# Performance work log

Measured on AMD Instinct MI355X. Metric: run time of the kernel, lower is better.

Reference implementation:

```python
import jax, jax.numpy as jnp
import numpy as np

FEAT_STRIDE = 16
SCORE_THRESH = 0.7
DIST_THRESH = 16.0
MAX_OUT = 50
B = 2048
IMG_W = 65536


def setup_inputs() -> dict:
    key = jax.random.key(0)
    k1, k2, k3 = jax.random.split(key, 3)
    fw = IMG_W // FEAT_STRIDE
    pred_cls_logit = jax.random.normal(k1, (B, fw), dtype=jnp.float32)
    pred_delta = jax.random.normal(k2, (B, fw, 2), dtype=jnp.float32)
    # realistic image widths in [0.5, 1.0] * img_width
    real_images_width = jax.random.uniform(k3, (B,), jnp.float32, 0.5, 1.0) * IMG_W
    return {
        "pred_cls_logit": pred_cls_logit,
        "pred_delta": pred_delta,
        "img_width": IMG_W,
        "real_images_width": real_images_width,
    }


def _nms_one(positions, scores):
    # positions: [N, 2], scores: [N]. Greedy 1D NMS, fixed MAX_OUT iterations.
    centers = positions.mean(axis=1)                      # [N]
    alive0 = scores >= SCORE_THRESH                       # score-threshold filter

    def step(alive, _):
        masked = jnp.where(alive, scores, -1e30)
        i = jnp.argmax(masked)                            # highest remaining score
        has = jnp.any(alive)
        f = has.astype(jnp.float32)                       # 1.0 if a box was picked
        p = positions[i] * f
        s = scores[i] * f
        # suppress everything within DIST_THRESH of picked center (incl. itself)
        new_alive = alive & (jnp.abs(centers - centers[i]) > DIST_THRESH)
        return new_alive, (p, s, f)

    _, (P, S, F) = jax.lax.scan(step, alive0, None, length=MAX_OUT)
    # pad_to_fixed_size: append validity flag column, zero-padded rows
    nms_positions = jnp.concatenate([P, F[:, None]], axis=1)   # [MAX_OUT, 3]
    nms_scores = jnp.concatenate([S[:, None], F[:, None]], axis=1)  # [MAX_OUT, 2]
    return nms_positions, nms_scores


def reference(pred_cls_logit, pred_delta, img_width, real_images_width):
    feat_width = img_width // FEAT_STRIDE
    interval_center = (jnp.arange(feat_width, dtype=jnp.float32) + 0.5) * FEAT_STRIDE
    # [B, feat_width, 2]
    pos = pred_delta * FEAT_STRIDE + interval_center[None, :, None]
    scores = jax.nn.sigmoid(pred_cls_logit)               # [B, feat_width]
    max_width = real_images_width[:, None, None] - 1.0
    pos = jnp.where(pos < 0.0, 0.0, pos)
    pos = jnp.where(pos > max_width, max_width, pos)

    nms_positions, nms_scores = jax.vmap(_nms_one)(pos, scores)

    nms_center = nms_positions[..., :2].mean(axis=2)      # [B, MAX_OUT]
    x_interval_num = jnp.floor(nms_center / FEAT_STRIDE).astype(jnp.int32)
    valid = nms_positions[..., 2] == 1.0
    idx = jnp.where(valid, x_interval_num, feat_width)    # out-of-range -> dropped
    cls_ids = jax.vmap(
        lambda ii: jnp.zeros((feat_width,), jnp.float32).at[ii].set(1.0, mode='drop')
    )(idx)                                                # [B, feat_width]
    return nms_positions, nms_scores, cls_ids
```

## Files before the change

kernel.cpp:

```cpp
#include <hip/hip_runtime.h>
#include <math.h>

#define FW 4096
#define MAX_OUT 50
#define WCAP 320
#define NSLOT 1024
#define T0 0.885f
#define SELCAP 128


__global__ __launch_bounds__(256) void essp_k1(
    const float* __restrict__ logits,
    const float* __restrict__ deltas,
    const float* __restrict__ realw,
    float* stage)
{
  __shared__ float Lx[4][WCAP];
  __shared__ int   Li[4][WCAP];
  __shared__ int   Lcnt[4];
  __shared__ int   Lsel, Lalv;

  const int row  = blockIdx.x;
  const int tid  = threadIdx.x;
  const int lane = tid & 63;
  const int w    = tid >> 6;

  if (tid == 0) { Lsel = 0; Lalv = 0; }

  const float mw = realw[row] - 1.0f;
  const float* lgr = logits + (size_t)row * FW;
  const float* dlr = deltas + (size_t)row * (2 * FW);
  const unsigned long long below = (1ULL << lane) - 1ULL;

  int cnt = 0;
  #pragma unroll
  for (int r = 0; r < 4; ++r) {
    const int i0 = w * 1024 + r * 256 + 4 * lane;
    const float4 lx = *(const float4*)(lgr + i0);
    const float xs[4] = {lx.x, lx.y, lx.z, lx.w};
    bool c4[4]; unsigned long long m4[4];
    #pragma unroll
    for (int e = 0; e < 4; ++e) { c4[e] = (xs[e] >= 0.846f); m4[e] = __ballot(c4[e]); }
    int base = cnt + __popcll(m4[0] & below) + __popcll(m4[1] & below)
                   + __popcll(m4[2] & below) + __popcll(m4[3] & below);
    int off = 0;
    #pragma unroll
    for (int e = 0; e < 4; ++e) {
      if (c4[e]) {
        const int slot = base + off;
        if (slot < WCAP) { Lx[w][slot] = xs[e]; Li[w][slot] = i0 + e; }
        ++off;
      }
    }
    cnt += __popcll(m4[0]) + __popcll(m4[1]) + __popcll(m4[2]) + __popcll(m4[3]);
  }
  if (lane == 0) Lcnt[w] = (cnt < WCAP) ? cnt : WCAP;
  __syncthreads();

  const int c0 = Lcnt[0], c1 = Lcnt[1], c2 = Lcnt[2], c3 = Lcnt[3];
  const int p1 = c0, p2 = c0 + c1, p3 = c0 + c1 + c2;
  int nc = p3 + c3; nc = (nc < NSLOT) ? nc : NSLOT;

  float* Srow = stage + (size_t)row * FW;
  unsigned short* idxrow = (unsigned short*)(Srow + 2048);
  unsigned long long* keyrow = (unsigned long long*)(Srow + 2560);

  #pragma unroll
  for (int g0 = 0; g0 < NSLOT; g0 += 256) {
    const int g = g0 + tid;
    float score = -1e30f, cen = 0.0f;
    int idx = 0;
    if (g < nc) {
      const int wsel = (g >= p1) + (g >= p2) + (g >= p3);
      int pre = 0;
      pre = (wsel == 1) ? p1 : pre;
      pre = (wsel == 2) ? p2 : pre;
      pre = (wsel == 3) ? p3 : pre;
      const int kk = g - pre;
      const float x = (&Lx[0][0])[wsel * WCAP + kk];
      idx = (&Li[0][0])[wsel * WCAP + kk];
      const float2 d = *(const float2*)(dlr + 2 * idx);
      const float ic = ((float)idx + 0.5f) * 16.0f;
      float q0 = d.x * 16.0f + ic;
      float q1 = d.y * 16.0f + ic;
      q0 = (q0 < 0.f) ? 0.f : q0;  q0 = (q0 > mw) ? mw : q0;
      q1 = (q1 < 0.f) ? 0.f : q1;  q1 = (q1 > mw) ? mw : q1;
      cen = (q0 + q1) * 0.5f;
      const float s = (float)(1.0 / (1.0 + exp(-(double)x)));
      score = (s >= 0.7f) ? s : -1e30f;
    }
    Srow[g]        = score;
    Srow[1024 + g] = cen;
    idxrow[g]      = (unsigned short)idx;

    const unsigned long long am = __ballot(score >= 0.7f);
    if (lane == 0) atomicAdd(&Lalv, __popcll(am));
    const unsigned long long sm = __ballot(score >= T0);
    int sbase = 0;
    if (lane == 0 && sm) sbase = atomicAdd(&Lsel, __popcll(sm));
    sbase = __shfl(sbase, 0, 64);
    if (score >= T0) {
      const int pos = sbase + __popcll(sm & below);
      if (pos < SELCAP) {
        keyrow[pos] = (((unsigned long long)__float_as_uint(score)) << 11)
                      | (unsigned)(2047 - g);
        Srow[2816 + pos] = cen;
      }
    }
  }
  __syncthreads();
  if (tid == 0) {
    *(int*)(Srow + 2944) = Lsel;
    *(int*)(Srow + 2945) = Lalv;
  }
}

#define KDEF(J, SS, CE)                                                       \
  const unsigned kb##J = ((SS) >= 0.7f) ? __float_as_uint(SS) : 0u;           \
  const float c##J = (CE);

#define INIT1F(J, SLOTEXPR)                                                   \
  unsigned long long fk##J = kb##J                                            \
      ? ((((unsigned long long)kb##J) << 11) | (unsigned)(2047 - (SLOTEXPR))) \
      : 0ULL;

#define M2(RK, RC, KA, CA, KB, CB)                                            \
  const bool t##RK = (KB) > (KA);                                             \
  const unsigned long long RK = t##RK ? (KB) : (KA);                          \
  const float RC = t##RK ? (CB) : (CA);

#define BSTEP(CTRL) {                                                         \
  const unsigned lo_ = (unsigned)__builtin_amdgcn_update_dpp(                 \
      (int)(unsigned)bk, (int)(unsigned)bk, CTRL, 0xF, 0xF, false);           \
  const unsigned hi_ = (unsigned)__builtin_amdgcn_update_dpp(                 \
      (int)(unsigned)(bk >> 32), (int)(unsigned)(bk >> 32), CTRL, 0xF, 0xF,   \
      false);                                                                 \
  const float oc_ = __int_as_float(__builtin_amdgcn_update_dpp(               \
      __float_as_int(bc), __float_as_int(bc), CTRL, 0xF, 0xF, false));        \
  const unsigned long long ok_ = ((unsigned long long)hi_ << 32) | lo_;       \
  const bool tb_ = ok_ > bk;                                                  \
  bk = tb_ ? ok_ : bk;  bc = tb_ ? oc_ : bc; }

#define SUPF(J) {                                                             \
  const bool ts_ = fabsf(c##J - wc) <= 16.0f;                                 \
  fk##J = ts_ ? 0ULL : fk##J; }

__global__ __launch_bounds__(64) void essp_k2(
    const float* __restrict__ deltas,
    const float* __restrict__ realw,
    float* out_pos,
    float* out_scr,
    float* cls_all)
{
  const int row  = blockIdx.x;
  const int lane = threadIdx.x;
  const int l4   = 4 * lane;
  float* Srow = cls_all + (size_t)row * FW;

  const int sel = *(const int*)(Srow + 2944);
  const int alv = *(const int*)(Srow + 2945);

  int pkv = -1;
  float psv = 0.f;
  bool need_heavy = (sel > SELCAP);

  if (!need_heavy) {
    const unsigned long long* kp = (const unsigned long long*)(Srow + 2560);
    unsigned long long ka = (lane < sel)      ? kp[lane]      : 0ULL;
    unsigned long long kb = (lane + 64 < sel) ? kp[lane + 64] : 0ULL;
    const float ca = (lane < sel)      ? Srow[2816 + lane]      : 0.f;
    const float cb = (lane + 64 < sel) ? Srow[2816 + 64 + lane] : 0.f;

    int cacc = 0;
    #pragma unroll 1
    for (int it = 0; it < MAX_OUT; ++it) {
      const bool tm = kb > ka;
      unsigned long long bk = tm ? kb : ka;
      float bc = tm ? cb : ca;
      BSTEP(0xB1)
      BSTEP(0x4E)
      BSTEP(0x141)
      BSTEP(0x140)
      BSTEP(0x142)
      BSTEP(0x143)
      const unsigned rhi = (unsigned)__builtin_amdgcn_readlane(
          (int)(unsigned)(bk >> 32), 63);
      const unsigned rlo = (unsigned)__builtin_amdgcn_readlane(
          (int)(unsigned)bk, 63);
      const float rc = __int_as_float(
          __builtin_amdgcn_readlane(__float_as_int(bc), 63));
      const unsigned sbits = (rhi << 21) | (rlo >> 11);
      if (sbits == 0u) break;
      if (lane == it) {
        pkv = 2047 - (int)(rlo & 0x7FFu);
        psv = __uint_as_float(sbits);
      }
      ++cacc;
      const float wc = rc;
      if (fabsf(ca - wc) <= 16.0f) ka = 0ULL;
      if (fabsf(cb - wc) <= 16.0f) kb = 0ULL;
    }
    if (cacc < MAX_OUT && alv > sel) { need_heavy = true; pkv = -1; psv = 0.f; }
  }

  if (need_heavy) {
    const float4 s4a = *(const float4*)(Srow + l4);
    const float4 s4b = *(const float4*)(Srow + 256 + l4);
    const float4 s4c = *(const float4*)(Srow + 512 + l4);
    const float4 s4d = *(const float4*)(Srow + 768 + l4);
    const float4 e4a = *(const float4*)(Srow + 1024 + l4);
    const float4 e4b = *(const float4*)(Srow + 1280 + l4);
    const float4 e4c = *(const float4*)(Srow + 1536 + l4);
    const float4 e4d = *(const float4*)(Srow + 1792 + l4);

    KDEF(0,  s4a.x, e4a.x)  KDEF(1,  s4a.y, e4a.y)
    KDEF(2,  s4a.z, e4a.z)  KDEF(3,  s4a.w, e4a.w)
    KDEF(4,  s4b.x, e4b.x)  KDEF(5,  s4b.y, e4b.y)
    KDEF(6,  s4b.z, e4b.z)  KDEF(7,  s4b.w, e4b.w)
    KDEF(8,  s4c.x, e4c.x)  KDEF(9,  s4c.y, e4c.y)
    KDEF(10, s4c.z, e4c.z)  KDEF(11, s4c.w, e4c.w)
    KDEF(12, s4d.x, e4d.x)  KDEF(13, s4d.y, e4d.y)
    KDEF(14, s4d.z, e4d.z)  KDEF(15, s4d.w, e4d.w)

    INIT1F(0,  l4 + 0)       INIT1F(1,  l4 + 1)       INIT1F(2,  l4 + 2)
    INIT1F(3,  l4 + 3)       INIT1F(4,  256 + l4 + 0) INIT1F(5,  256 + l4 + 1)
    INIT1F(6,  256 + l4 + 2) INIT1F(7,  256 + l4 + 3) INIT1F(8,  512 + l4 + 0)
    INIT1F(9,  512 + l4 + 1) INIT1F(10, 512 + l4 + 2) INIT1F(11, 512 + l4 + 3)
    INIT1F(12, 768 + l4 + 0) INIT1F(13, 768 + l4 + 1) INIT1F(14, 768 + l4 + 2)
    INIT1F(15, 768 + l4 + 3)

    #pragma unroll 1
    for (int it = 0; it < MAX_OUT; ++it) {
      M2(ka0, ca0, fk0,  c0,  fk1,  c1)
      M2(ka1, ca1, fk2,  c2,  fk3,  c3)
      M2(ka2, ca2, fk4,  c4,  fk5,  c5)
      M2(ka3, ca3, fk6,  c6,  fk7,  c7)
      M2(ka4, ca4, fk8,  c8,  fk9,  c9)
      M2(ka5, ca5, fk10, c10, fk11, c11)
      M2(ka6, ca6, fk12, c12, fk13, c13)
      M2(ka7, ca7, fk14, c14, fk15, c15)
      M2(kb0, cb0, ka0, ca0, ka1, ca1)
      M2(kb1, cb1, ka2, ca2, ka3, ca3)
      M2(kb2, cb2, ka4, ca4, ka5, ca5)
      M2(kb3, cb3, ka6, ca6, ka7, ca7)
      M2(kc0, cc0, kb0, cb0, kb1, cb1)
      M2(kc1, cc1, kb2, cb2, kb3, cb3)
      M2(kd0, cd0, kc0, cc0, kc1, cc1)

      unsigned long long bk = kd0;
      float bc = cd0;
      BSTEP(0xB1) BSTEP(0x4E) BSTEP(0x141) BSTEP(0x140) BSTEP(0x142) BSTEP(0x143)

      const unsigned rhi = (unsigned)__builtin_amdgcn_readlane(
          (int)(unsigned)(bk >> 32), 63);
      const unsigned rlo = (unsigned)__builtin_amdgcn_readlane(
          (int)(unsigned)bk, 63);
      const float rc = __int_as_float(
          __builtin_amdgcn_readlane(__float_as_int(bc), 63));
      const unsigned sbits = (rhi << 21) | (rlo >> 11);
      const bool valid = sbits != 0u;
      const float wc = valid ? rc : 3.0e38f;
      if (lane == it) {
        pkv = valid ? (2047 - (int)(rlo & 0x7FFu)) : -1;
        psv = __uint_as_float(sbits);
      }
      SUPF(0)  SUPF(1)  SUPF(2)  SUPF(3)  SUPF(4)  SUPF(5)  SUPF(6)  SUPF(7)
      SUPF(8)  SUPF(9)  SUPF(10) SUPF(11) SUPF(12) SUPF(13) SUPF(14) SUPF(15)
    }
  }

  float p0 = 0.f, p1 = 0.f;
  int ci = -1;
  if (pkv >= 0) {
    const int idx = ((const unsigned short*)(Srow + 2048))[pkv];
    const float2 d = *(const float2*)(deltas + (size_t)row * (2 * FW) + 2 * idx);
    const float mw = realw[row] - 1.0f;
    const float ic = ((float)idx + 0.5f) * 16.0f;
    p0 = d.x * 16.0f + ic;
    p1 = d.y * 16.0f + ic;
    p0 = (p0 < 0.f) ? 0.f : p0;  p0 = (p0 > mw) ? mw : p0;
    p1 = (p1 < 0.f) ? 0.f : p1;  p1 = (p1 > mw) ? mw : p1;
    ci = (int)floorf(((p0 + p1) * 0.5f) * 0.0625f);
  }
  asm volatile("s_waitcnt vmcnt(0)" ::: "memory");

  const float4 z4 = make_float4(0.f, 0.f, 0.f, 0.f);
  #pragma unroll
  for (int q = 0; q < 16; ++q)
    *(float4*)(Srow + 256 * q + l4) = z4;
  asm volatile("s_waitcnt vmcnt(0)" ::: "memory");

  float* prow = out_pos + (size_t)row * (MAX_OUT * 3);
  float* srow = out_scr + (size_t)row * (MAX_OUT * 2);
  if (lane < MAX_OUT) {
    if (pkv >= 0) {
      prow[3 * lane + 0] = p0;
      prow[3 * lane + 1] = p1;
      prow[3 * lane + 2] = 1.0f;
      srow[2 * lane + 0] = psv;
      srow[2 * lane + 1] = 1.0f;
      if (ci >= 0 && ci < FW) Srow[ci] = 1.0f;
    } else {
      prow[3 * lane + 0] = 0.0f;
      prow[3 * lane + 1] = 0.0f;
      prow[3 * lane + 2] = 0.0f;
      srow[2 * lane + 0] = 0.0f;
      srow[2 * lane + 1] = 0.0f;
    }
  }
}

extern "C" void kernel_launch(void* const* d_in, const int* in_sizes, int n_in,
                              void* d_out, int out_size, void* d_ws, size_t ws_size,
                              hipStream_t stream) {
  const float* logits = (const float*)d_in[0];
  const float* deltas = (const float*)d_in[1];
  const float* realw  = (const float*)d_in[3];
  const int Bn = in_sizes[3];
  float* out_pos = (float*)d_out;
  float* out_scr = out_pos + (size_t)Bn * MAX_OUT * 3;
  float* out_cls = out_scr + (size_t)Bn * MAX_OUT * 2;

  essp_k1<<<Bn, 256, 0, stream>>>(logits, deltas, realw, out_cls);
  essp_k2<<<Bn, 64, 0, stream>>>(deltas, realw, out_pos, out_scr, out_cls);
}
```

Baseline: 77.23 us.

## Fuse candidate-extraction and NMS kernels into one block using shared memory

Merges the two kernels so that scores, centers, indices and the selection keys stay in LDS instead of being staged through the cls output buffer in global memory. The cls row is zeroed at kernel start, and only wave 0 goes on to run the greedy NMS after the barrier. This removes a launch, the global staging round trip and the separate zeroing pass after NMS. In exchange, LDS per block grows, which may lower occupancy, and three of the four waves sit idle during the serial NMS phase.

New measurement: 84.14 us. 9.0% more time.

```diff
diff --git a/kernel.cpp b/kernel.cpp
--- a/kernel.cpp
+++ b/kernel.cpp
@@ -8,17 +8,53 @@
 #define T0 0.885f
 #define SELCAP 128
 
-
-__global__ __launch_bounds__(256) void essp_k1(
+#define KDEF(J, SS, CE)                                                       \
+  const unsigned kb##J = ((SS) >= 0.7f) ? __float_as_uint(SS) : 0u;           \
+  const float c##J = (CE);
+
+#define INIT1F(J, SLOTEXPR)                                                   \
+  unsigned long long fk##J = kb##J                                            \
+      ? ((((unsigned long long)kb##J) << 11) | (unsigned)(2047 - (SLOTEXPR))) \
+      : 0ULL;
+
+#define M2(RK, RC, KA, CA, KB, CB)                                            \
+  const bool t##RK = (KB) > (KA);                                             \
+  const unsigned long long RK = t##RK ? (KB) : (KA);                          \
+  const float RC = t##RK ? (CB) : (CA);
+
+#define BSTEP(CTRL) {                                                         \
+  const unsigned lo_ = (unsigned)__builtin_amdgcn_update_dpp(                 \
+      (int)(unsigned)bk, (int)(unsigned)bk, CTRL, 0xF, 0xF, false);           \
+  const unsigned hi_ = (unsigned)__builtin_amdgcn_update_dpp(                 \
+      (int)(unsigned)(bk >> 32), (int)(unsigned)(bk >> 32), CTRL, 0xF, 0xF,   \
+      false);                                                                 \
+  const float oc_ = __int_as_float(__builtin_amdgcn_update_dpp(               \
+      __float_as_int(bc), __float_as_int(bc), CTRL, 0xF, 0xF, false));        \
+  const unsigned long long ok_ = ((unsigned long long)hi_ << 32) | lo_;       \
+  const bool tb_ = ok_ > bk;                                                  \
+  bk = tb_ ? ok_ : bk;  bc = tb_ ? oc_ : bc; }
+
+#define SUPF(J) {                                                             \
+  const bool ts_ = fabsf(c##J - wc) <= 16.0f;                                 \
+  fk##J = ts_ ? 0ULL : fk##J; }
+
+__global__ __launch_bounds__(256) void essp_fused(
     const float* __restrict__ logits,
     const float* __restrict__ deltas,
     const float* __restrict__ realw,
-    float* stage)
+    float* __restrict__ out_pos,
+    float* __restrict__ out_scr,
+    float* __restrict__ out_cls)
 {
   __shared__ float Lx[4][WCAP];
   __shared__ int   Li[4][WCAP];
   __shared__ int   Lcnt[4];
-  __shared__ int   Lsel, Lalv;
+  __shared__ __align__(16) float Lsc[NSLOT];
+  __shared__ __align__(16) float Lce[NSLOT];
+  __shared__ unsigned short Lidx[NSLOT];
+  __shared__ unsigned long long Lkey[SELCAP];
+  __shared__ float Lc2[SELCAP];
+  __shared__ int Lsel, Lalv;
 
   const int row  = blockIdx.x;
   const int tid  = threadIdx.x;
@@ -30,7 +66,14 @@
   const float mw = realw[row] - 1.0f;
   const float* lgr = logits + (size_t)row * FW;
   const float* dlr = deltas + (size_t)row * (2 * FW);
+  float* cls = out_cls + (size_t)row * FW;
   const unsigned long long below = (1ULL << lane) - 1ULL;
+
+  {
+    const float4 z = make_float4(0.f, 0.f, 0.f, 0.f);
+    #pragma unroll
+    for (int r = 0; r < 4; ++r) *(float4*)(cls + 1024 * r + 4 * tid) = z;
+  }
 
   int cnt = 0;
   #pragma unroll
@@ -58,12 +101,8 @@
   __syncthreads();
 
   const int c0 = Lcnt[0], c1 = Lcnt[1], c2 = Lcnt[2], c3 = Lcnt[3];
-  const int p1 = c0, p2 = c0 + c1, p3 = c0 + c1 + c2;
-  int nc = p3 + c3; nc = (nc < NSLOT) ? nc : NSLOT;
-
-  float* Srow = stage + (size_t)row * FW;
-  unsigned short* idxrow = (unsigned short*)(Srow + 2048);
-  unsigned long long* keyrow = (unsigned long long*)(Srow + 2560);
+  const int pw1 = c0, pw2 = c0 + c1, pw3 = c0 + c1 + c2;
+  int nc = pw3 + c3; nc = (nc < NSLOT) ? nc : NSLOT;
 
   #pragma unroll
   for (int g0 = 0; g0 < NSLOT; g0 += 256) {
@@ -71,11 +110,11 @@
     float score = -1e30f, cen = 0.0f;
     int idx = 0;
     if (g < nc) {
-      const int wsel = (g >= p1) + (g >= p2) + (g >= p3);
+      const int wsel = (g >= pw1) + (g >= pw2) + (g >= pw3);
       int pre = 0;
-      pre = (wsel == 1) ? p1 : pre;
-      pre = (wsel == 2) ? p2 : pre;
-      pre = (wsel == 3) ? p3 : pre;
+      pre = (wsel == 1) ? pw1 : pre;
+      pre = (wsel == 2) ? pw2 : pre;
+      pre = (wsel == 3) ? pw3 : pre;
       const int kk = g - pre;
       const float x = (&Lx[0][0])[wsel * WCAP + kk];
       idx = (&Li[0][0])[wsel * WCAP + kk];
@@ -89,9 +128,9 @@
       const float s = (float)(1.0 / (1.0 + exp(-(double)x)));
       score = (s >= 0.7f) ? s : -1e30f;
     }
-    Srow[g]        = score;
-    Srow[1024 + g] = cen;
-    idxrow[g]      = (unsigned short)idx;
+    Lsc[g]  = score;
+    Lce[g]  = cen;
+    Lidx[g] = (unsigned short)idx;
 
     const unsigned long long am = __ballot(score >= 0.7f);
     if (lane == 0) atomicAdd(&Lalv, __popcll(am));
@@ -102,74 +141,25 @@
     if (score >= T0) {
       const int pos = sbase + __popcll(sm & below);
       if (pos < SELCAP) {
-        keyrow[pos] = (((unsigned long long)__float_as_uint(score)) << 11)
-                      | (unsigned)(2047 - g);
-        Srow[2816 + pos] = cen;
+        Lkey[pos] = (((unsigned long long)__float_as_uint(score)) << 11)
+                    | (unsigned)(2047 - g);
+        Lc2[pos] = cen;
       }
     }
   }
   __syncthreads();
-  if (tid == 0) {
-    *(int*)(Srow + 2944) = Lsel;
-    *(int*)(Srow + 2945) = Lalv;
-  }
-}
-
-#define KDEF(J, SS, CE)                                                       \
-  const unsigned kb##J = ((SS) >= 0.7f) ? __float_as_uint(SS) : 0u;           \
-  const float c##J = (CE);
-
-#define INIT1F(J, SLOTEXPR)                                                   \
-  unsigned long long fk##J = kb##J                                            \
-      ? ((((unsigned long long)kb##J) << 11) | (unsigned)(2047 - (SLOTEXPR))) \
-      : 0ULL;
-
-#define M2(RK, RC, KA, CA, KB, CB)                                            \
-  const bool t##RK = (KB) > (KA);                                             \
-  const unsigned long long RK = t##RK ? (KB) : (KA);                          \
-  const float RC = t##RK ? (CB) : (CA);
-
-#define BSTEP(CTRL) {                                                         \
-  const unsigned lo_ = (unsigned)__builtin_amdgcn_update_dpp(                 \
-      (int)(unsigned)bk, (int)(unsigned)bk, CTRL, 0xF, 0xF, false);           \
-  const unsigned hi_ = (unsigned)__builtin_amdgcn_update_dpp(                 \
-      (int)(unsigned)(bk >> 32), (int)(unsigned)(bk >> 32), CTRL, 0xF, 0xF,   \
-      false);                                                                 \
-  const float oc_ = __int_as_float(__builtin_amdgcn_update_dpp(               \
-      __float_as_int(bc), __float_as_int(bc), CTRL, 0xF, 0xF, false));        \
-  const unsigned long long ok_ = ((unsigned long long)hi_ << 32) | lo_;       \
-  const bool tb_ = ok_ > bk;                                                  \
-  bk = tb_ ? ok_ : bk;  bc = tb_ ? oc_ : bc; }
-
-#define SUPF(J) {                                                             \
-  const bool ts_ = fabsf(c##J - wc) <= 16.0f;                                 \
-  fk##J = ts_ ? 0ULL : fk##J; }
-
-__global__ __launch_bounds__(64) void essp_k2(
-    const float* __restrict__ deltas,
-    const float* __restrict__ realw,
-    float* out_pos,
-    float* out_scr,
-    float* cls_all)
-{
-  const int row  = blockIdx.x;
-  const int lane = threadIdx.x;
-  const int l4   = 4 * lane;
-  float* Srow = cls_all + (size_t)row * FW;
-
-  const int sel = *(const int*)(Srow + 2944);
-  const int alv = *(const int*)(Srow + 2945);
-
+  if (w != 0) return;
+
+  const int sel = Lsel, alv = Lalv;
   int pkv = -1;
   float psv = 0.f;
   bool need_heavy = (sel > SELCAP);
 
   if (!need_heavy) {
-    const unsigned long long* kp = (const unsigned long long*)(Srow + 2560);
-    unsigned long long ka = (lane < sel)      ? kp[lane]      : 0ULL;
-    unsigned long long kb = (lane + 64 < sel) ? kp[lane + 64] : 0ULL;
-    const float ca = (lane < sel)      ? Srow[2816 + lane]      : 0.f;
-    const float cb = (lane + 64 < sel) ? Srow[2816 + 64 + lane] : 0.f;
+    unsigned long long ka = (lane < sel)      ? Lkey[lane]      : 0ULL;
+    unsigned long long kb = (lane + 64 < sel) ? Lkey[lane + 64] : 0ULL;
+    const float ca = (lane < sel)      ? Lc2[lane]      : 0.f;
+    const float cb = (lane + 64 < sel) ? Lc2[lane + 64] : 0.f;
 
     int cacc = 0;
     #pragma unroll 1
@@ -204,14 +194,15 @@
   }
 
   if (need_heavy) {
-    const float4 s4a = *(const float4*)(Srow + l4);
-    const float4 s4b = *(const float4*)(Srow + 256 + l4);
-    const float4 s4c = *(const float4*)(Srow + 512 + l4);
-    const float4 s4d = *(const float4*)(Srow + 768 + l4);
-    const float4 e4a = *(const float4*)(Srow + 1024 + l4);
-    const float4 e4b = *(const float4*)(Srow + 1280 + l4);
-    const float4 e4c = *(const float4*)(Srow + 1536 + l4);
-    const float4 e4d = *(const float4*)(Srow + 1792 + l4);
+    const int l4 = 4 * lane;
+    const float4 s4a = *(const float4*)(&Lsc[l4]);
+    const float4 s4b = *(const float4*)(&Lsc[256 + l4]);
+    const float4 s4c = *(const float4*)(&Lsc[512 + l4]);
+    const float4 s4d = *(const float4*)(&Lsc[768 + l4]);
+    const float4 e4a = *(const float4*)(&Lce[l4]);
+    const float4 e4b = *(const float4*)(&Lce[256 + l4]);
+    const float4 e4c = *(const float4*)(&Lce[512 + l4]);
+    const float4 e4d = *(const float4*)(&Lce[768 + l4]);
 
     KDEF(0,  s4a.x, e4a.x)  KDEF(1,  s4a.y, e4a.y)
     KDEF(2,  s4a.z, e4a.z)  KDEF(3,  s4a.w, e4a.w)
@@ -269,37 +260,29 @@
     }
   }
 
-  float p0 = 0.f, p1 = 0.f;
+  float q0 = 0.f, q1 = 0.f;
   int ci = -1;
-  if (pkv >= 0) {
-    const int idx = ((const unsigned short*)(Srow + 2048))[pkv];
-    const float2 d = *(const float2*)(deltas + (size_t)row * (2 * FW) + 2 * idx);
-    const float mw = realw[row] - 1.0f;
+  if (lane < MAX_OUT && pkv >= 0) {
+    const int idx = Lidx[pkv];
+    const float2 d = *(const float2*)(dlr + 2 * idx);
     const float ic = ((float)idx + 0.5f) * 16.0f;
-    p0 = d.x * 16.0f + ic;
-    p1 = d.y * 16.0f + ic;
-    p0 = (p0 < 0.f) ? 0.f : p0;  p0 = (p0 > mw) ? mw : p0;
-    p1 = (p1 < 0.f) ? 0.f : p1;  p1 = (p1 > mw) ? mw : p1;
-    ci = (int)floorf(((p0 + p1) * 0.5f) * 0.0625f);
-  }
-  asm volatile("s_waitcnt vmcnt(0)" ::: "memory");
-
-  const float4 z4 = make_float4(0.f, 0.f, 0.f, 0.f);
-  #pragma unroll
-  for (int q = 0; q < 16; ++q)
-    *(float4*)(Srow + 256 * q + l4) = z4;
-  asm volatile("s_waitcnt vmcnt(0)" ::: "memory");
+    q0 = d.x * 16.0f + ic;
+    q1 = d.y * 16.0f + ic;
+    q0 = (q0 < 0.f) ? 0.f : q0;  q0 = (q0 > mw) ? mw : q0;
+    q1 = (q1 < 0.f) ? 0.f : q1;  q1 = (q1 > mw) ? mw : q1;
+    ci = (int)floorf(((q0 + q1) * 0.5f) * 0.0625f);
+  }
 
   float* prow = out_pos + (size_t)row * (MAX_OUT * 3);
   float* srow = out_scr + (size_t)row * (MAX_OUT * 2);
   if (lane < MAX_OUT) {
     if (pkv >= 0) {
-      prow[3 * lane + 0] = p0;
-      prow[3 * lane + 1] = p1;
+      prow[3 * lane + 0] = q0;
+      prow[3 * lane + 1] = q1;
       prow[3 * lane + 2] = 1.0f;
       srow[2 * lane + 0] = psv;
       srow[2 * lane + 1] = 1.0f;
-      if (ci >= 0 && ci < FW) Srow[ci] = 1.0f;
+      if (ci >= 0 && ci < FW) cls[ci] = 1.0f;
     } else {
       prow[3 * lane + 0] = 0.0f;
       prow[3 * lane + 1] = 0.0f;
@@ -321,6 +304,6 @@
   float* out_scr = out_pos + (size_t)Bn * MAX_OUT * 3;
   float* out_cls = out_scr + (size_t)Bn * MAX_OUT * 2;
 
-  essp_k1<<<Bn, 256, 0, stream>>>(logits, deltas, realw, out_cls);
-  essp_k2<<<Bn, 64, 0, stream>>>(deltas, realw, out_pos, out_scr, out_cls);
+  essp_fused<<<Bn, 256, 0, stream>>>(logits, deltas, realw,
+                                     out_pos, out_scr, out_cls);
 }
```

## Pack NMS keys to 32 bits and interleave four rows per wave

Applied to the files above, without the earlier changes.

Candidate keys shrink from 64-bit to 32-bit by storing the score offset above the threshold bits plus a 10-bit slot, which halves the DPP max-reduction work per step. The second kernel now handles four rows per 64-lane block and interleaves their independent NMS loops so the DPP/readlane latency chains overlap. The heavy fallback moves into a noinline function that runs only after the light pass. The light loop no longer exits early and always runs 50 iterations per row, and the grid has four times fewer blocks, which may reduce occupancy.

New measurement: 147.5 us. +91.0%, slower.

```diff
diff --git a/kernel.cpp b/kernel.cpp
--- a/kernel.cpp
+++ b/kernel.cpp
@@ -6,6 +6,7 @@
 #define WCAP 320
 #define NSLOT 1024
 #define T0 0.885f
+#define T0BITS 0x3F628F5Cu
 #define SELCAP 128
 
 
@@ -63,7 +64,7 @@
 
   float* Srow = stage + (size_t)row * FW;
   unsigned short* idxrow = (unsigned short*)(Srow + 2048);
-  unsigned long long* keyrow = (unsigned long long*)(Srow + 2560);
+  unsigned* keyrow = (unsigned*)(Srow + 2560);
 
   #pragma unroll
   for (int g0 = 0; g0 < NSLOT; g0 += 256) {
@@ -102,9 +103,9 @@
     if (score >= T0) {
       const int pos = sbase + __popcll(sm & below);
       if (pos < SELCAP) {
-        keyrow[pos] = (((unsigned long long)__float_as_uint(score)) << 11)
-                      | (unsigned)(2047 - g);
-        Srow[2816 + pos] = cen;
+        keyrow[pos] = ((__float_as_uint(score) - T0BITS + 1u) << 10)
+                      | (unsigned)(1023 - g);
+        Srow[2688 + pos] = cen;
       }
     }
   }
@@ -145,169 +146,191 @@
   const bool ts_ = fabsf(c##J - wc) <= 16.0f;                                 \
   fk##J = ts_ ? 0ULL : fk##J; }
 
+struct PR { int pkv; float psv; };
+
+__device__ __attribute__((noinline)) PR heavy_nms(const float* Srow, int lane) {
+  const int l4 = 4 * lane;
+  const float4 s4a = *(const float4*)(Srow + l4);
+  const float4 s4b = *(const float4*)(Srow + 256 + l4);
+  const float4 s4c = *(const float4*)(Srow + 512 + l4);
+  const float4 s4d = *(const float4*)(Srow + 768 + l4);
+  const float4 e4a = *(const float4*)(Srow + 1024 + l4);
+  const float4 e4b = *(const float4*)(Srow + 1280 + l4);
+  const float4 e4c = *(const float4*)(Srow + 1536 + l4);
+  const float4 e4d = *(const float4*)(Srow + 1792 + l4);
+
+  KDEF(0,  s4a.x, e4a.x)  KDEF(1,  s4a.y, e4a.y)
+  KDEF(2,  s4a.z, e4a.z)  KDEF(3,  s4a.w, e4a.w)
+  KDEF(4,  s4b.x, e4b.x)  KDEF(5,  s4b.y, e4b.y)
+  KDEF(6,  s4b.z, e4b.z)  KDEF(7,  s4b.w, e4b.w)
+  KDEF(8,  s4c.x, e4c.x)  KDEF(9,  s4c.y, e4c.y)
+  KDEF(10, s4c.z, e4c.z)  KDEF(11, s4c.w, e4c.w)
+  KDEF(12, s4d.x, e4d.x)  KDEF(13, s4d.y, e4d.y)
+  KDEF(14, s4d.z, e4d.z)  KDEF(15, s4d.w, e4d.w)
+
+  INIT1F(0,  l4 + 0)       INIT1F(1,  l4 + 1)       INIT1F(2,  l4 + 2)
+  INIT1F(3,  l4 + 3)       INIT1F(4,  256 + l4 + 0) INIT1F(5,  256 + l4 + 1)
+  INIT1F(6,  256 + l4 + 2) INIT1F(7,  256 + l4 + 3) INIT1F(8,  512 + l4 + 0)
+  INIT1F(9,  512 + l4 + 1) INIT1F(10, 512 + l4 + 2) INIT1F(11, 512 + l4 + 3)
+  INIT1F(12, 768 + l4 + 0) INIT1F(13, 768 + l4 + 1) INIT1F(14, 768 + l4 + 2)
+  INIT1F(15, 768 + l4 + 3)
+
+  int pkv = -1; float psv = 0.f;
+  #pragma unroll 1
+  for (int it = 0; it < MAX_OUT; ++it) {
+    M2(ka0, ca0, fk0,  c0,  fk1,  c1)
+    M2(ka1, ca1, fk2,  c2,  fk3,  c3)
+    M2(ka2, ca2, fk4,  c4,  fk5,  c5)
+    M2(ka3, ca3, fk6,  c6,  fk7,  c7)
+    M2(ka4, ca4, fk8,  c8,  fk9,  c9)
+    M2(ka5, ca5, fk10, c10, fk11, c11)
+    M2(ka6, ca6, fk12, c12, fk13, c13)
+    M2(ka7, ca7, fk14, c14, fk15, c15)
+    M2(kb0, cb0, ka0, ca0, ka1, ca1)
+    M2(kb1, cb1, ka2, ca2, ka3, ca3)
+    M2(kb2, cb2, ka4, ca4, ka5, ca5)
+    M2(kb3, cb3, ka6, ca6, ka7, ca7)
+    M2(kc0, cc0, kb0, cb0, kb1, cb1)
+    M2(kc1, cc1, kb2, cb2, kb3, cb3)
+    M2(kd0, cd0, kc0, cc0, kc1, cc1)
+
+    unsigned long long bk = kd0;
+    float bc = cd0;
+    BSTEP(0xB1) BSTEP(0x4E) BSTEP(0x141) BSTEP(0x140) BSTEP(0x142) BSTEP(0x143)
+
+    const unsigned rhi = (unsigned)__builtin_amdgcn_readlane(
+        (int)(unsigned)(bk >> 32), 63);
+    const unsigned rlo = (unsigned)__builtin_amdgcn_readlane(
+        (int)(unsigned)bk, 63);
+    const float rc = __int_as_float(
+        __builtin_amdgcn_readlane(__float_as_int(bc), 63));
+    const unsigned sbits = (rhi << 21) | (rlo >> 11);
+    const bool valid = sbits != 0u;
+    const float wc = valid ? rc : 3.0e38f;
+    if (lane == it) {
+      pkv = valid ? (2047 - (int)(rlo & 0x7FFu)) : -1;
+      psv = __uint_as_float(sbits);
+    }
+    SUPF(0)  SUPF(1)  SUPF(2)  SUPF(3)  SUPF(4)  SUPF(5)  SUPF(6)  SUPF(7)
+    SUPF(8)  SUPF(9)  SUPF(10) SUPF(11) SUPF(12) SUPF(13) SUPF(14) SUPF(15)
+  }
+  PR r; r.pkv = pkv; r.psv = psv; return r;
+}
+
+#define BST32(CTRL) {                                                         \
+  const unsigned ok_ = (unsigned)__builtin_amdgcn_update_dpp(                 \
+      (int)bk, (int)bk, CTRL, 0xF, 0xF, false);                               \
+  const float oc_ = __int_as_float(__builtin_amdgcn_update_dpp(               \
+      __float_as_int(bc), __float_as_int(bc), CTRL, 0xF, 0xF, false));        \
+  const bool tb_ = ok_ > bk;                                                  \
+  bk = tb_ ? ok_ : bk;  bc = tb_ ? oc_ : bc; }
+
+#define ROWSETUP(R)                                                           \
+  float* Srow##R = cls_all + (size_t)(row0 + R) * FW;                         \
+  const bool rv##R = (row0 + R) < Bn;                                         \
+  const int sel##R = rv##R ? *(const int*)(Srow##R + 2944) : 0;               \
+  const int alv##R = rv##R ? *(const int*)(Srow##R + 2945) : 0;               \
+  const unsigned* kp##R = (const unsigned*)(Srow##R + 2560);                  \
+  unsigned ka##R = (lane < sel##R)      ? kp##R[lane]      : 0u;              \
+  unsigned kb##R = (lane + 64 < sel##R) ? kp##R[lane + 64] : 0u;              \
+  const float ca##R = (lane < sel##R)      ? Srow##R[2688 + lane]      : 0.f; \
+  const float cb##R = (lane + 64 < sel##R) ? Srow##R[2688 + 64 + lane] : 0.f; \
+  int pkv##R = -1; float psv##R = 0.f; int cacc##R = 0;
+
+#define NMSROW(R) {                                                           \
+  const bool tm_ = kb##R > ka##R;                                             \
+  unsigned bk = tm_ ? kb##R : ka##R;                                          \
+  float bc = tm_ ? cb##R : ca##R;                                             \
+  BST32(0xB1) BST32(0x4E) BST32(0x141) BST32(0x140) BST32(0x142) BST32(0x143) \
+  const unsigned rk_ = (unsigned)__builtin_amdgcn_readlane((int)bk, 63);      \
+  const float rc_ = __int_as_float(                                           \
+      __builtin_amdgcn_readlane(__float_as_int(bc), 63));                     \
+  const bool valid_ = (rk_ != 0u);                                            \
+  cacc##R += valid_ ? 1 : 0;                                                  \
+  if (lane == it && valid_) {                                                 \
+    pkv##R = 1023 - (int)(rk_ & 1023u);                                       \
+    psv##R = __uint_as_float(((rk_ >> 10) - 1u) + T0BITS);                    \
+  }                                                                           \
+  const float wc_ = valid_ ? rc_ : 3.0e38f;                                   \
+  if (fabsf(ca##R - wc_) <= 16.0f) ka##R = 0u;                                \
+  if (fabsf(cb##R - wc_) <= 16.0f) kb##R = 0u;                                \
+}
+
+#define FBCHK(R)                                                              \
+  if (rv##R && ((sel##R > SELCAP) ||                                          \
+                (cacc##R < MAX_OUT && alv##R > sel##R))) {                    \
+    const PR pr_ = heavy_nms(Srow##R, lane);                                  \
+    pkv##R = pr_.pkv; psv##R = pr_.psv;                                       \
+  }
+
+#define GATH(R)                                                               \
+  float q0##R = 0.f, q1##R = 0.f; int ci##R = -1;                             \
+  if (lane < MAX_OUT && pkv##R >= 0) {                                        \
+    const int idx_ = ((const unsigned short*)(Srow##R + 2048))[pkv##R];       \
+    const float2 d_ = *(const float2*)(deltas + (size_t)(row0 + R) * (2 * FW) \
+                                       + 2 * idx_);                           \
+    const float mw_ = realw[row0 + R] - 1.0f;                                 \
+    const float ic_ = ((float)idx_ + 0.5f) * 16.0f;                           \
+    q0##R = d_.x * 16.0f + ic_;  q1##R = d_.y * 16.0f + ic_;                  \
+    q0##R = (q0##R < 0.f) ? 0.f : q0##R; q0##R = (q0##R > mw_) ? mw_ : q0##R; \
+    q1##R = (q1##R < 0.f) ? 0.f : q1##R; q1##R = (q1##R > mw_) ? mw_ : q1##R; \
+    ci##R = (int)floorf(((q0##R + q1##R) * 0.5f) * 0.0625f);                  \
+  }
+
+#define ZROW(R)                                                               \
+  if (rv##R) {                                                                \
+    for (int q = 0; q < 16; ++q)                                              \
+      *(float4*)(Srow##R + 256 * q + 4 * lane) = z4;                          \
+  }
+
+#define OUTW(R)                                                               \
+  if (rv##R && lane < MAX_OUT) {                                              \
+    float* prow_ = out_pos + (size_t)(row0 + R) * (MAX_OUT * 3);              \
+    float* srow_ = out_scr + (size_t)(row0 + R) * (MAX_OUT * 2);              \
+    if (pkv##R >= 0) {                                                        \
+      prow_[3 * lane + 0] = q0##R;                                            \
+      prow_[3 * lane + 1] = q1##R;                                            \
+      prow_[3 * lane + 2] = 1.0f;                                             \
+      srow_[2 * lane + 0] = psv##R;                                           \
+      srow_[2 * lane + 1] = 1.0f;                                             \
+      if (ci##R >= 0 && ci##R < FW) Srow##R[ci##R] = 1.0f;                    \
+    } else {                                                                  \
+      prow_[3 * lane + 0] = 0.0f;                                             \
+      prow_[3 * lane + 1] = 0.0f;                                             \
+      prow_[3 * lane + 2] = 0.0f;                                             \
+      srow_[2 * lane + 0] = 0.0f;                                             \
+      srow_[2 * lane + 1] = 0.0f;                                             \
+    }                                                                         \
+  }
+
 __global__ __launch_bounds__(64) void essp_k2(
     const float* __restrict__ deltas,
     const float* __restrict__ realw,
     float* out_pos,
     float* out_scr,
-    float* cls_all)
+    float* cls_all,
+    int Bn)
 {
-  const int row  = blockIdx.x;
   const int lane = threadIdx.x;
-  const int l4   = 4 * lane;
-  float* Srow = cls_all + (size_t)row * FW;
-
-  const int sel = *(const int*)(Srow + 2944);
-  const int alv = *(const int*)(Srow + 2945);
-
-  int pkv = -1;
-  float psv = 0.f;
-  bool need_heavy = (sel > SELCAP);
-
-  if (!need_heavy) {
-    const unsigned long long* kp = (const unsigned long long*)(Srow + 2560);
-    unsigned long long ka = (lane < sel)      ? kp[lane]      : 0ULL;
-    unsigned long long kb = (lane + 64 < sel) ? kp[lane + 64] : 0ULL;
-    const float ca = (lane < sel)      ? Srow[2816 + lane]      : 0.f;
-    const float cb = (lane + 64 < sel) ? Srow[2816 + 64 + lane] : 0.f;
-
-    int cacc = 0;
-    #pragma unroll 1
-    for (int it = 0; it < MAX_OUT; ++it) {
-      const bool tm = kb > ka;
-      unsigned long long bk = tm ? kb : ka;
-      float bc = tm ? cb : ca;
-      BSTEP(0xB1)
-      BSTEP(0x4E)
-      BSTEP(0x141)
-      BSTEP(0x140)
-      BSTEP(0x142)
-      BSTEP(0x143)
-      const unsigned rhi = (unsigned)__builtin_amdgcn_readlane(
-          (int)(unsigned)(bk >> 32), 63);
-      const unsigned rlo = (unsigned)__builtin_amdgcn_readlane(
-          (int)(unsigned)bk, 63);
-      const float rc = __int_as_float(
-          __builtin_amdgcn_readlane(__float_as_int(bc), 63));
-      const unsigned sbits = (rhi << 21) | (rlo >> 11);
-      if (sbits == 0u) break;
-      if (lane == it) {
-        pkv = 2047 - (int)(rlo & 0x7FFu);
-        psv = __uint_as_float(sbits);
-      }
-      ++cacc;
-      const float wc = rc;
-      if (fabsf(ca - wc) <= 16.0f) ka = 0ULL;
-      if (fabsf(cb - wc) <= 16.0f) kb = 0ULL;
-    }
-    if (cacc < MAX_OUT && alv > sel) { need_heavy = true; pkv = -1; psv = 0.f; }
-  }
-
-  if (need_heavy) {
-    const float4 s4a = *(const float4*)(Srow + l4);
-    const float4 s4b = *(const float4*)(Srow + 256 + l4);
-    const float4 s4c = *(const float4*)(Srow + 512 + l4);
-    const float4 s4d = *(const float4*)(Srow + 768 + l4);
-    const float4 e4a = *(const float4*)(Srow + 1024 + l4);
-    const float4 e4b = *(const float4*)(Srow + 1280 + l4);
-    const float4 e4c = *(const float4*)(Srow + 1536 + l4);
-    const float4 e4d = *(const float4*)(Srow + 1792 + l4);
-
-    KDEF(0,  s4a.x, e4a.x)  KDEF(1,  s4a.y, e4a.y)
-    KDEF(2,  s4a.z, e4a.z)  KDEF(3,  s4a.w, e4a.w)
-    KDEF(4,  s4b.x, e4b.x)  KDEF(5,  s4b.y, e4b.y)
-    KDEF(6,  s4b.z, e4b.z)  KDEF(7,  s4b.w, e4b.w)
-    KDEF(8,  s4c.x, e4c.x)  KDEF(9,  s4c.y, e4c.y)
-    KDEF(10, s4c.z, e4c.z)  KDEF(11, s4c.w, e4c.w)
-    KDEF(12, s4d.x, e4d.x)  KDEF(13, s4d.y, e4d.y)
-    KDEF(14, s4d.z, e4d.z)  KDEF(15, s4d.w, e4d.w)
-
-    INIT1F(0,  l4 + 0)       INIT1F(1,  l4 + 1)       INIT1F(2,  l4 + 2)
-    INIT1F(3,  l4 + 3)       INIT1F(4,  256 + l4 + 0) INIT1F(5,  256 + l4 + 1)
-    INIT1F(6,  256 + l4 + 2) INIT1F(7,  256 + l4 + 3) INIT1F(8,  512 + l4 + 0)
-    INIT1F(9,  512 + l4 + 1) INIT1F(10, 512 + l4 + 2) INIT1F(11, 512 + l4 + 3)
-    INIT1F(12, 768 + l4 + 0) INIT1F(13, 768 + l4 + 1) INIT1F(14, 768 + l4 + 2)
-    INIT1F(15, 768 + l4 + 3)
-
-    #pragma unroll 1
-    for (int it = 0; it < MAX_OUT; ++it) {
-      M2(ka0, ca0, fk0,  c0,  fk1,  c1)
-      M2(ka1, ca1, fk2,  c2,  fk3,  c3)
-      M2(ka2, ca2, fk4,  c4,  fk5,  c5)
-      M2(ka3, ca3, fk6,  c6,  fk7,  c7)
-      M2(ka4, ca4, fk8,  c8,  fk9,  c9)
-      M2(ka5, ca5, fk10, c10, fk11, c11)
-      M2(ka6, ca6, fk12, c12, fk13, c13)
-      M2(ka7, ca7, fk14, c14, fk15, c15)
-      M2(kb0, cb0, ka0, ca0, ka1, ca1)
-      M2(kb1, cb1, ka2, ca2, ka3, ca3)
-      M2(kb2, cb2, ka4, ca4, ka5, ca5)
-      M2(kb3, cb3, ka6, ca6, ka7, ca7)
-      M2(kc0, cc0, kb0, cb0, kb1, cb1)
-      M2(kc1, cc1, kb2, cb2, kb3, cb3)
-      M2(kd0, cd0, kc0, cc0, kc1, cc1)
-
-      unsigned long long bk = kd0;
-      float bc = cd0;
-      BSTEP(0xB1) BSTEP(0x4E) BSTEP(0x141) BSTEP(0x140) BSTEP(0x142) BSTEP(0x143)
-
-      const unsigned rhi = (unsigned)__builtin_amdgcn_readlane(
-          (int)(unsigned)(bk >> 32), 63);
-      const unsigned rlo = (unsigned)__builtin_amdgcn_readlane(
-          (int)(unsigned)bk, 63);
-      const float rc = __int_as_float(
-          __builtin_amdgcn_readlane(__float_as_int(bc), 63));
-      const unsigned sbits = (rhi << 21) | (rlo >> 11);
-      const bool valid = sbits != 0u;
-      const float wc = valid ? rc : 3.0e38f;
-      if (lane == it) {
-        pkv = valid ? (2047 - (int)(rlo & 0x7FFu)) : -1;
-        psv = __uint_as_float(sbits);
-      }
-      SUPF(0)  SUPF(1)  SUPF(2)  SUPF(3)  SUPF(4)  SUPF(5)  SUPF(6)  SUPF(7)
-      SUPF(8)  SUPF(9)  SUPF(10) SUPF(11) SUPF(12) SUPF(13) SUPF(14) SUPF(15)
-    }
-  }
-
-  float p0 = 0.f, p1 = 0.f;
-  int ci = -1;
-  if (pkv >= 0) {
-    const int idx = ((const unsigned short*)(Srow + 2048))[pkv];
-    const float2 d = *(const float2*)(deltas + (size_t)row * (2 * FW) + 2 * idx);
-    const float mw = realw[row] - 1.0f;
-    const float ic = ((float)idx + 0.5f) * 16.0f;
-    p0 = d.x * 16.0f + ic;
-    p1 = d.y * 16.0f + ic;
-    p0 = (p0 < 0.f) ? 0.f : p0;  p0 = (p0 > mw) ? mw : p0;
-    p1 = (p1 < 0.f) ? 0.f : p1;  p1 = (p1 > mw) ? mw : p1;
-    ci = (int)floorf(((p0 + p1) * 0.5f) * 0.0625f);
-  }
+  const int row0 = blockIdx.x * 4;
+
+  ROWSETUP(0) ROWSETUP(1) ROWSETUP(2) ROWSETUP(3)
+
+  #pragma unroll 1
+  for (int it = 0; it < MAX_OUT; ++it) {
+    NMSROW(0) NMSROW(1) NMSROW(2) NMSROW(3)
+  }
+
+  FBCHK(0) FBCHK(1) FBCHK(2) FBCHK(3)
+
+  GATH(0) GATH(1) GATH(2) GATH(3)
   asm volatile("s_waitcnt vmcnt(0)" ::: "memory");
 
   const float4 z4 = make_float4(0.f, 0.f, 0.f, 0.f);
-  #pragma unroll
-  for (int q = 0; q < 16; ++q)
-    *(float4*)(Srow + 256 * q + l4) = z4;
+  ZROW(0) ZROW(1) ZROW(2) ZROW(3)
   asm volatile("s_waitcnt vmcnt(0)" ::: "memory");
 
-  float* prow = out_pos + (size_t)row * (MAX_OUT * 3);
-  float* srow = out_scr + (size_t)row * (MAX_OUT * 2);
-  if (lane < MAX_OUT) {
-    if (pkv >= 0) {
-      prow[3 * lane + 0] = p0;
-      prow[3 * lane + 1] = p1;
-      prow[3 * lane + 2] = 1.0f;
-      srow[2 * lane + 0] = psv;
-      srow[2 * lane + 1] = 1.0f;
-      if (ci >= 0 && ci < FW) Srow[ci] = 1.0f;
-    } else {
-      prow[3 * lane + 0] = 0.0f;
-      prow[3 * lane + 1] = 0.0f;
-      prow[3 * lane + 2] = 0.0f;
-      srow[2 * lane + 0] = 0.0f;
-      srow[2 * lane + 1] = 0.0f;
-    }
-  }
+  OUTW(0) OUTW(1) OUTW(2) OUTW(3)
 }
 
 extern "C" void kernel_launch(void* const* d_in, const int* in_sizes, int n_in,
@@ -322,5 +345,6 @@
   float* out_cls = out_scr + (size_t)Bn * MAX_OUT * 2;
 
   essp_k1<<<Bn, 256, 0, stream>>>(logits, deltas, realw, out_cls);
-  essp_k2<<<Bn, 64, 0, stream>>>(deltas, realw, out_pos, out_scr, out_cls);
-}
+  essp_k2<<<(Bn + 3) / 4, 64, 0, stream>>>(deltas, realw,
+                                           out_pos, out_scr, out_cls, Bn);
+}
```
